# Performance work log

Measured on AMD Instinct MI355X. Metric: run time of the kernel, lower is better.

The kernel has to match this reference:

```python
import jax, jax.numpy as jnp
import numpy as np

# Config matching init_kwargs
C, H_IMG, W_IMG = 3, 224, 224
N_PATCHES = 14
PS = H_IMG // N_PATCHES            # 16
INPUT_D = C * PS * PS              # 768
HID = 768
N_HEADS = 12
DH = HID // N_HEADS                # 64
N_BLOCKS = 12
MLP_RATIO = 4
SEQ = N_PATCHES * N_PATCHES + 1    # 197
EPS = 1e-5


def _pos_embed():
    # sin on even dims, cos on odd dims, exponent uses (j - j%2)/d  (faithful to loop)
    i = jnp.arange(SEQ, dtype=jnp.float32)[:, None]
    j = jnp.arange(HID, dtype=jnp.float32)[None, :]
    expo = (j - jnp.mod(j, 2.0)) / HID
    ang = i / jnp.power(10000.0, expo)
    return jnp.where(jnp.mod(jnp.arange(HID), 2) == 0, jnp.sin(ang), jnp.cos(ang))


def setup_inputs() -> dict:
    key = jax.random.key(0)
    ks = jax.random.split(key, 16)
    s = 0.02
    d_ff = MLP_RATIO * HID
    inp = {
        'images': jax.random.normal(ks[0], (16, C, H_IMG, W_IMG), dtype=jnp.float32),
        'w_map': jax.random.normal(ks[1], (HID, INPUT_D), dtype=jnp.float32) * s,
        'b_map': jnp.zeros((HID,), dtype=jnp.float32),
        'class_token': jax.random.uniform(ks[2], (1, HID), dtype=jnp.float32),
        'pos_embed': _pos_embed(),
        'qw': jax.random.normal(ks[3], (N_BLOCKS, N_HEADS, DH, DH), dtype=jnp.float32) * s,
        'qb': jnp.zeros((N_BLOCKS, N_HEADS, DH), dtype=jnp.float32),
        'kw': jax.random.normal(ks[4], (N_BLOCKS, N_HEADS, DH, DH), dtype=jnp.float32) * s,
        'kb': jnp.zeros((N_BLOCKS, N_HEADS, DH), dtype=jnp.float32),
        'vw': jax.random.normal(ks[5], (N_BLOCKS, N_HEADS, DH, DH), dtype=jnp.float32) * s,
        'vb': jnp.zeros((N_BLOCKS, N_HEADS, DH), dtype=jnp.float32),
        'ln1_w': jnp.ones((N_BLOCKS, HID), dtype=jnp.float32),
        'ln1_b': jnp.zeros((N_BLOCKS, HID), dtype=jnp.float32),
        'ln2_w': jnp.ones((N_BLOCKS, HID), dtype=jnp.float32),
        'ln2_b': jnp.zeros((N_BLOCKS, HID), dtype=jnp.float32),
        'mlp_w1': jax.random.normal(ks[6], (N_BLOCKS, d_ff, HID), dtype=jnp.float32) * s,
        'mlp_b1': jnp.zeros((N_BLOCKS, d_ff), dtype=jnp.float32),
        'mlp_w2': jax.random.normal(ks[7], (N_BLOCKS, HID, d_ff), dtype=jnp.float32) * s,
        'mlp_b2': jnp.zeros((N_BLOCKS, HID), dtype=jnp.float32),
    }
    return inp


def _layernorm(x, w, b):
    mu = jnp.mean(x, axis=-1, keepdims=True)
    var = jnp.mean(jnp.square(x - mu), axis=-1, keepdims=True)
    return (x - mu) * jax.lax.rsqrt(var + EPS) * w + b


def _patchify(images):
    # [N,C,H,W] -> [N, np^2, C*ps*ps]; per-patch flatten order is (c, ph, pw)
    n = images.shape[0]
    x = images.reshape(n, C, N_PATCHES, PS, N_PATCHES, PS)
    x = x.transpose(0, 2, 4, 1, 3, 5)  # n, pi, pj, c, ph, pw
    return x.reshape(n, N_PATCHES * N_PATCHES, INPUT_D)


def _msa(x, qw, qb, kw, kb, vw, vb):
    # x: [B,S,D]; per-head Linear on head slices; torch Linear: y = x @ W.T + b
    b_, s_, _ = x.shape
    xh = x.reshape(b_, s_, N_HEADS, DH)
    q = jnp.einsum('bshd,hod->bsho', xh, qw) + qb
    k = jnp.einsum('bshd,hod->bsho', xh, kw) + kb
    v = jnp.einsum('bshd,hod->bsho', xh, vw) + vb
    attn = jax.nn.softmax(jnp.einsum('bsho,btho->bhst', q, k) / (DH ** 0.5), axis=-1)
    out = jnp.einsum('bhst,btho->bsho', attn, v)
    return out.reshape(b_, s_, HID)


def reference(images, w_map, b_map, class_token, pos_embed, qw, qb, kw, kb, vw, vb,
              ln1_w, ln1_b, ln2_w, ln2_b, mlp_w1, mlp_b1, mlp_w2, mlp_b2):
    patches = _patchify(images)                       # [N, 196, 768]
    tokens = patches @ w_map.T + b_map                # [N, 196, HID]
    n = tokens.shape[0]
    cls = jnp.broadcast_to(class_token[None], (n, 1, HID))
    out = jnp.concatenate([cls, tokens], axis=1) + pos_embed[None]  # [N, SEQ, HID]
    for l in range(N_BLOCKS):
        out = out + _msa(_layernorm(out, ln1_w[l], ln1_b[l]),
                         qw[l], qb[l], kw[l], kb[l], vw[l], vb[l])
        h = _layernorm(out, ln2_w[l], ln2_b[l])
        h = jax.nn.gelu(h @ mlp_w1[l].T + mlp_b1[l], approximate=False)
        out = out + (h @ mlp_w2[l].T + mlp_b2[l])
    return out
```

## Files before the change

### kernel.cpp

```cpp
#include <hip/hip_runtime.h>
#include <hip/hip_bf16.h>
#include <math.h>

typedef __attribute__((ext_vector_type(4))) float f32x4;
typedef __attribute__((ext_vector_type(8))) __bf16 bf16x8;
typedef __attribute__((ext_vector_type(8))) short short8;
typedef __attribute__((ext_vector_type(4))) unsigned short us4;
typedef __attribute__((ext_vector_type(8))) unsigned short us8;

#define B_    16
#define SEQ_  197
#define TOK_  3152
#define HID_  768
#define MPAD_ 3200
#define NP_   3136
#define DFF_  3072
#define PSZ_  (MPAD_ * HID_)
#define QKVP_ 14336
#define BHN_  192

__device__ __forceinline__ unsigned short f2bf(float x) {
  union { float f; unsigned int u; } v; v.f = x;
  unsigned int r = v.u + 0x7fffu + ((v.u >> 16) & 1u);
  return (unsigned short)(r >> 16);
}

__device__ __forceinline__ float bf2f(unsigned short u) {
  union { unsigned int i; float f; } v; v.i = ((unsigned int)u) << 16; return v.f;
}

__device__ __forceinline__ f32x4 mfma16(bf16x8 a, bf16x8 b, f32x4 c) {
  return __builtin_amdgcn_mfma_f32_16x16x32_bf16(a, b, c, 0, 0, 0);
}

__device__ __forceinline__ void cp16(const void* g, void* l) {
  __builtin_amdgcn_global_load_lds((__attribute__((address_space(1))) void*)(g),
                                   (__attribute__((address_space(3))) void*)(l),
                                   16, 0, 0);
}

__device__ __forceinline__ float gelu_f(float x) {
  float y = x * (1.5957691216f + 0.0713548162f * x * x);
  float e = __expf(y);
  float r = 1.0f / (1.0f + e);
  return x - x * r;
}

__device__ __forceinline__ void conv8(const float* __restrict__ s, unsigned short* __restrict__ d, int c) {
  const float* sp = s + (size_t)c * 8;
  f32x4 v0 = *(const f32x4*)sp;
  f32x4 v1 = *(const f32x4*)(sp + 4);
  us8 o;
  o[0] = f2bf(v0[0]); o[1] = f2bf(v0[1]); o[2] = f2bf(v0[2]); o[3] = f2bf(v0[3]);
  o[4] = f2bf(v1[0]); o[5] = f2bf(v1[1]); o[6] = f2bf(v1[2]); o[7] = f2bf(v1[3]);
  *(us8*)(d + (size_t)c * 8) = o;
}

__global__ __launch_bounds__(256) void patchcls_kernel(const float* __restrict__ img,
                                                       unsigned short* __restrict__ Pb,
                                                       const float* __restrict__ ct,
                                                       const float* __restrict__ pos,
                                                       float* __restrict__ X,
                                                       const float* __restrict__ wmap,
                                                       unsigned short* __restrict__ Wmb,
                                                       const float* __restrict__ cw1,
                                                       unsigned short* __restrict__ cd1,
                                                       const float* __restrict__ cw2,
                                                       unsigned short* __restrict__ cd2) {
  int bid = blockIdx.x;
  if (bid >= 2736) {
    int bb = bid - 2736;
    const float* s; unsigned short* d;
    if (bb < 1152) { s = cw1; d = cd1; } else { s = cw2; d = cd2; bb -= 1152; }
    conv8(s, d, bb * 256 + threadIdx.x);
    return;
  }
  if (bid >= 2448) {
    int c = (bid - 2448) * 256 + threadIdx.x;
    conv8(wmap, Wmb, c);
    return;
  }
  if (bid >= 2400) {
    int j = (bid - 2400) * 256 + threadIdx.x;
    if (j < B_ * HID_) {
      int b = j / HID_, t = j - b * HID_;
      X[(size_t)b * SEQ_ * HID_ + t] = ct[t] + pos[t];
    }
    return;
  }
  int gid = bid * 256 + threadIdx.x;
  int m = gid / 192;
  int j4 = (gid - m * 192) * 4;
  us4 o;
  if (m < NP_) {
    int n = m / 196, p = m - n * 196;
    int pi = p / 14, pj = p - pi * 14;
    int c = j4 >> 8, rem = j4 & 255, ph = rem >> 4, pw = rem & 15;
    const float* src = img + (((size_t)(n * 3 + c) * 224 + pi * 16 + ph) * 224 + pj * 16 + pw);
    f32x4 v = *(const f32x4*)src;
    o[0] = f2bf(v[0]); o[1] = f2bf(v[1]); o[2] = f2bf(v[2]); o[3] = f2bf(v[3]);
  } else {
    o[0] = 0; o[1] = 0; o[2] = 0; o[3] = 0;
  }
  *(us4*)(Pb + (size_t)m * HID_ + j4) = o;
}

__global__ __launch_bounds__(256) void convw_kernel(const float* __restrict__ s1, unsigned short* __restrict__ d1,
                                                    const float* __restrict__ s2, unsigned short* __restrict__ d2,
                                                    int nchunks) {
  int half = gridDim.x >> 1;
  int b = blockIdx.x;
  const float* s; unsigned short* d;
  if (b < half) { s = s1; d = d1; } else { s = s2; d = d2; b -= half; }
  int c = b * 256 + threadIdx.x;
  if (c >= nchunks) return;
  conv8(s, d, c);
}

__global__ __launch_bounds__(256) void gemm_embed(const unsigned short* __restrict__ A,
                                                  const unsigned short* __restrict__ Bw,
                                                  const float* __restrict__ bias,
                                                  const float* __restrict__ pos,
                                                  float* __restrict__ Xout) {
  constexpr int MI = 2, NJ = 2, BM = 64, BN = 64;
  __shared__ unsigned short As[BM * 64];
  __shared__ unsigned short Bs[BN * 64];
  const int tid = threadIdx.x;
  const int w = tid >> 6, lane = tid & 63;
  const int lr = lane & 15, kg = lane >> 4;
  int bid = blockIdx.x;
  int cpx = gridDim.x >> 3;
  int swz = (bid & 7) * cpx + (bid >> 3);
  const int by = swz / 12, bx = swz - by * 12;
  const int m0 = by * BM, n0 = bx * BN;
  const int wr = w >> 1, wc = w & 1;
  const f32x4 z4 = {0.f, 0.f, 0.f, 0.f};
  f32x4 acc[MI][NJ];
#pragma unroll
  for (int i = 0; i < MI; ++i)
#pragma unroll
    for (int j = 0; j < NJ; ++j) acc[i][j] = z4;
  for (int k0 = 0; k0 < 768; k0 += 64) {
#pragma unroll
    for (int is = 0; is < MI; ++is) {
      int chunk = is * 256 + tid;
      int row = chunk >> 3, cc = (chunk & 7) * 8;
      cp16(A + (size_t)(m0 + row) * 768 + k0 + cc, As + is * 2048 + w * 512);
    }
#pragma unroll
    for (int is = 0; is < NJ; ++is) {
      int chunk = is * 256 + tid;
      int row = chunk >> 3, cc = (chunk & 7) * 8;
      cp16(Bw + (size_t)(n0 + row) * 768 + k0 + cc, Bs + is * 2048 + w * 512);
    }
    __syncthreads();
#pragma unroll
    for (int kk = 0; kk < 64; kk += 32) {
      bf16x8 af[MI], bfr[NJ];
#pragma unroll
      for (int i = 0; i < MI; ++i)
        af[i] = *(const bf16x8*)&As[(wr * (BM / 2) + i * 16 + lr) * 64 + kk + kg * 8];
#pragma unroll
      for (int j = 0; j < NJ; ++j)
        bfr[j] = *(const bf16x8*)&Bs[(wc * (BN / 2) + j * 16 + lr) * 64 + kk + kg * 8];
#pragma unroll
      for (int i = 0; i < MI; ++i)
#pragma unroll
        for (int j = 0; j < NJ; ++j)
          acc[i][j] = mfma16(af[i], bfr[j], acc[i][j]);
    }
    __syncthreads();
  }
#pragma unroll
  for (int i = 0; i < MI; ++i) {
    int mbase = m0 + wr * (BM / 2) + i * 16 + kg * 4;
#pragma unroll
    for (int j = 0; j < NJ; ++j) {
      int col = n0 + wc * (BN / 2) + j * 16 + lr;
#pragma unroll
      for (int qr = 0; qr < 4; ++qr) {
        int m = mbase + qr;
        if (m < NP_) {
          int nimg = m / 196;
          int tok = m + nimg + 1;
          int prow = m - nimg * 196 + 1;
          Xout[(size_t)tok * HID_ + col] = acc[i][j][qr] + bias[col] + pos[(size_t)prow * HID_ + col];
        }
      }
    }
  }
}

template<int EPI, int NT>
__global__ __launch_bounds__(256, 3) void gemm4b(const unsigned short* __restrict__ A,
                                                 const unsigned short* __restrict__ Bw,
                                                 int ldk, int gx, int gy,
                                                 const float* __restrict__ bias,
                                                 unsigned short* __restrict__ Pout,
                                                 unsigned short* __restrict__ Hout) {
  __shared__ unsigned short lds3[24576];
  const int tid = threadIdx.x;
  const int wid = tid >> 6, lane = tid & 63;
  const int lr = lane & 15, kg = lane >> 4;
  const int wm = wid >> 1, wn = wid & 1;
  const int nwg = gridDim.x;
  const int q = nwg >> 3, r = nwg & 7;
  const int xcd = blockIdx.x & 7, idx = blockIdx.x >> 3;
  const int wgid = (xcd < r ? xcd * (q + 1) : r * (q + 1) + (xcd - r) * q) + idx;
  const int bx = wgid % gx;
  const int rest = wgid / gx;
  const int by = rest % gy;
  const int z = rest / gy;
  const int m0 = by * 128, n0 = bx * 128;
  const unsigned short* Abase = A + (size_t)m0 * ldk + z * (NT * 32);
  const unsigned short* Bbase = Bw + (size_t)n0 * ldk + z * (NT * 32);

  const int r0 = tid >> 2, u0 = tid & 3;
  const int r1 = 64 + r0;
  const int sk0 = (u0 ^ ((r0 >> 1) & 3)) * 8;
  const int sk1 = (u0 ^ ((r1 >> 1) & 3)) * 8;
  const int d0 = wid * 512;
  const int d1 = 2048 + wid * 512;

#pragma unroll
  for (int t = 0; t < 2; ++t) {
    unsigned short* lb = lds3 + t * 8192;
    cp16(Abase + (size_t)r0 * ldk + sk0 + t * 32, lb + d0);
    cp16(Abase + (size_t)r1 * ldk + sk1 + t * 32, lb + d1);
    cp16(Bbase + (size_t)r0 * ldk + sk0 + t * 32, lb + 4096 + d0);
    cp16(Bbase + (size_t)r1 * ldk + sk1 + t * 32, lb + 4096 + d1);
  }

  int offA[4], offB[4];
#pragma unroll
  for (int i = 0; i < 4; ++i) {
    int ra_ = wm * 64 + i * 16 + lr;
    offA[i] = ra_ * 32 + ((kg ^ ((ra_ >> 1) & 3)) * 8);
    int rb_ = wn * 64 + i * 16 + lr;
    offB[i] = rb_ * 32 + ((kg ^ ((rb_ >> 1) & 3)) * 8);
  }

  const f32x4 z4 = {0.f, 0.f, 0.f, 0.f};
  f32x4 acc[4][4];
#pragma unroll
  for (int i = 0; i < 4; ++i)
#pragma unroll
    for (int j = 0; j < 4; ++j) acc[i][j] = z4;

  int cur = 0;
#pragma unroll 1
  for (int k = 0; k < NT; ++k) {
    asm volatile("s_waitcnt vmcnt(4)" ::: "memory");
    __builtin_amdgcn_s_barrier();
    __builtin_amdgcn_sched_barrier(0);
    const unsigned short* lp = lds3 + cur * 8192;
    const int wb = (cur == 0) ? 2 : cur - 1;
    const int tn = k + 2;
    const int ts = (tn >= NT) ? tn - NT : tn;
    unsigned short* tb = lds3 + wb * 8192;
    bf16x8 af[4], bfr[4];
#pragma unroll
    for (int i = 0; i < 4; ++i)
      af[i] = *(const bf16x8*)(lp + offA[i]);
#pragma unroll
    for (int j = 0; j < 4; ++j)
      bfr[j] = *(const bf16x8*)(lp + 4096 + offB[j]);
    cp16(Abase + (size_t)r0 * ldk + sk0 + ts * 32, tb + d0);
    cp16(Abase + (size_t)r1 * ldk + sk1 + ts * 32, tb + d1);
    cp16(Bbase + (size_t)r0 * ldk + sk0 + ts * 32, tb + 4096 + d0);
    cp16(Bbase + (size_t)r1 * ldk + sk1 + ts * 32, tb + 4096 + d1);
    __builtin_amdgcn_s_setprio(1);
#pragma unroll
    for (int i = 0; i < 4; ++i)
#pragma unroll
      for (int j = 0; j < 4; ++j) acc[i][j] = mfma16(af[i], bfr[j], acc[i][j]);
    __builtin_amdgcn_s_setprio(0);
    cur = (cur == 2) ? 0 : cur + 1;
  }

#pragma unroll
  for (int i = 0; i < 4; ++i) {
    int mbase = m0 + wm * 64 + i * 16 + kg * 4;
#pragma unroll
    for (int j = 0; j < 4; ++j) {
      int col = n0 + wn * 64 + j * 16 + lr;
      float bv = (EPI == 1) ? bias[col] : 0.f;
#pragma unroll
      for (int qr = 0; qr < 4; ++qr) {
        int m = mbase + qr;
        if (m < TOK_) {
          float v = acc[i][j][qr];
          if (EPI == 1) {
            Hout[(size_t)m * 3072 + col] = f2bf(gelu_f(v + bv));
          } else {
            Pout[(size_t)z * PSZ_ + (size_t)m * 768 + col] = f2bf(v);
          }
        }
      }
    }
  }
}

template<int MODE>
__global__ __launch_bounds__(256) void ln_kernel(float* __restrict__ X,
                                                 const unsigned short* __restrict__ P, const float* __restrict__ pb,
                                                 const float* __restrict__ gw, const float* __restrict__ gb,
                                                 unsigned short* __restrict__ Y,
                                                 const float* __restrict__ cw1, unsigned short* __restrict__ cd1,
                                                 const float* __restrict__ cw2, unsigned short* __restrict__ cd2) {
  int bb = (int)blockIdx.x - 800;
  if (bb >= 0) {
    const float* s; unsigned short* d;
    if (bb < 1152) { s = cw1; d = cd1; } else { s = cw2; d = cd2; bb -= 1152; }
    conv8(s, d, bb * 256 + threadIdx.x);
    return;
  }
  int row = blockIdx.x * 4 + (threadIdx.x >> 6);
  int lane = threadIdx.x & 63;
  if (row >= MPAD_) return;
  size_t base = (size_t)row * HID_;
  if (row >= TOK_) {
    us4 zz; zz[0] = 0; zz[1] = 0; zz[2] = 0; zz[3] = 0;
#pragma unroll
    for (int i = 0; i < 3; ++i) *(us4*)(Y + base + i * 256 + lane * 4) = zz;
    return;
  }
  f32x4 xv[3];
  float s1 = 0.f, s2 = 0.f;
#pragma unroll
  for (int i = 0; i < 3; ++i) {
    int cb = i * 256 + lane * 4;
    f32x4 v = *(const f32x4*)(X + base + cb);
    if (MODE == 2) {
      const unsigned short* pp = P + base + cb;
      us4 p0 = *(const us4*)(pp);
      us4 p1 = *(const us4*)(pp + PSZ_);
      us4 p2 = *(const us4*)(pp + 2 * (size_t)PSZ_);
      us4 p3 = *(const us4*)(pp + 3 * (size_t)PSZ_);
      f32x4 bb2 = *(const f32x4*)(pb + cb);
#pragma unroll
      for (int e = 0; e < 4; ++e)
        v[e] += bf2f(p0[e]) + bf2f(p1[e]) + bf2f(p2[e]) + bf2f(p3[e]) + bb2[e];
      *(f32x4*)(X + base + cb) = v;
    }
    xv[i] = v;
    s1 += v[0] + v[1] + v[2] + v[3];
    s2 += v[0] * v[0] + v[1] * v[1] + v[2] * v[2] + v[3] * v[3];
  }
#pragma unroll
  for (int d = 1; d < 64; d <<= 1) {
    s1 += __shfl_xor(s1, d);
    s2 += __shfl_xor(s2, d);
  }
  float mu = s1 * (1.f / 768.f);
  float var = s2 * (1.f / 768.f) - mu * mu;
  float rs = rsqrtf(var + 1e-5f);
#pragma unroll
  for (int i = 0; i < 3; ++i) {
    int cb = i * 256 + lane * 4;
    us4 o;
#pragma unroll
    for (int e = 0; e < 4; ++e)
      o[e] = f2bf((xv[i][e] - mu) * rs * gw[cb + e] + gb[cb + e]);
    *(us4*)(Y + base + cb) = o;
  }
}

__global__ __launch_bounds__(256) void redfin_kernel(float* __restrict__ X, const unsigned short* __restrict__ P,
                                                     const float* __restrict__ b2) {
  int i = blockIdx.x * 256 + threadIdx.x;
  if (i >= TOK_ * 192) return;
  int m = i / 192, c4 = (i - m * 192) * 4;
  size_t off = (size_t)m * HID_ + c4;
  f32x4 v = *(const f32x4*)(X + off);
  const unsigned short* pp = P + off;
  us4 p0 = *(const us4*)(pp);
  us4 p1 = *(const us4*)(pp + PSZ_);
  us4 p2 = *(const us4*)(pp + 2 * (size_t)PSZ_);
  us4 p3 = *(const us4*)(pp + 3 * (size_t)PSZ_);
  f32x4 bb = *(const f32x4*)(b2 + c4);
#pragma unroll
  for (int e = 0; e < 4; ++e)
    v[e] += bf2f(p0[e]) + bf2f(p1[e]) + bf2f(p2[e]) + bf2f(p3[e]) + bb[e];
  *(f32x4*)(X + off) = v;
}

__device__ __forceinline__ void loadw_frags(const float* __restrict__ W, int lr, int kg, bf16x8* wf) {
#pragma unroll
  for (int j = 0; j < 4; ++j)
#pragma unroll
    for (int kk = 0; kk < 2; ++kk) {
      const float* wp = W + (j * 16 + lr) * 64 + kk * 32 + kg * 8;
      f32x4 w0 = *(const f32x4*)wp;
      f32x4 w1 = *(const f32x4*)(wp + 4);
      short8 t;
      t[0] = (short)f2bf(w0[0]); t[1] = (short)f2bf(w0[1]); t[2] = (short)f2bf(w0[2]); t[3] = (short)f2bf(w0[3]);
      t[4] = (short)f2bf(w1[0]); t[5] = (short)f2bf(w1[1]); t[6] = (short)f2bf(w1[2]); t[7] = (short)f2bf(w1[3]);
      wf[j * 2 + kk] = __builtin_bit_cast(bf16x8, t);
    }
}

__global__ __launch_bounds__(128) void qkvproj_kernel(const unsigned short* __restrict__ Y,
                                                      const float* __restrict__ qw, const float* __restrict__ qb,
                                                      const float* __restrict__ kw, const float* __restrict__ kb,
                                                      const float* __restrict__ vw, const float* __restrict__ vb,
                                                      unsigned short* __restrict__ Qo,
                                                      unsigned short* __restrict__ Ko,
                                                      unsigned short* __restrict__ Vto) {
  const int blk = blockIdx.x;
  const int half = blk & 1;
  const int bp = blk >> 1;
  const int p = bp % 3, bh = bp / 3;
  const int b = bh / 12, h = bh - b * 12;
  const int wv = threadIdx.x >> 6, lane = threadIdx.x & 63;
  const int lr = lane & 15, kg = lane >> 4;
  const int ws = half * 2 + wv;
  const float* W; const float* bs; unsigned short* out;
  if (p == 0)      { W = qw + h * 4096; bs = qb + h * 64; out = Qo; }
  else if (p == 1) { W = kw + h * 4096; bs = kb + h * 64; out = Ko; }
  else             { W = vw + h * 4096; bs = vb + h * 64; out = Vto; }
  const float scale = (p == 0) ? 0.125f : 1.0f;
  bf16x8 wf[8];
  loadw_frags(W, lr, kg, wf);
  float bj[4];
#pragma unroll
  for (int j = 0; j < 4; ++j) bj[j] = bs[j * 16 + lr];
  out += (size_t)bh * QKVP_;
  const f32x4 z4 = {0.f, 0.f, 0.f, 0.f};
  const short8 zs = {0, 0, 0, 0, 0, 0, 0, 0};
#pragma unroll
  for (int i = 0; i < 4; ++i) {
    int t = ws + 4 * i;
    if (t < 14) {
      int s = t * 16 + lr;
      bf16x8 a0 = __builtin_bit_cast(bf16x8, zs), a1 = a0;
      if (s < SEQ_) {
        const unsigned short* yp = Y + (size_t)(b * SEQ_ + s) * HID_ + h * 64 + kg * 8;
        a0 = *(const bf16x8*)yp;
        a1 = *(const bf16x8*)(yp + 32);
      }
      f32x4 acc[4] = {z4, z4, z4, z4};
#pragma unroll
      for (int j = 0; j < 4; ++j) {
        acc[j] = mfma16(a0, wf[j * 2 + 0], acc[j]);
        acc[j] = mfma16(a1, wf[j * 2 + 1], acc[j]);
      }
      if (p == 2) {
#pragma unroll
        for (int j = 0; j < 4; ++j) {
          us4 pk;
#pragma unroll
          for (int qr = 0; qr < 4; ++qr) {
            int srow = t * 16 + kg * 4 + qr;
            pk[qr] = (srow < SEQ_) ? f2bf(acc[j][qr] + bj[j]) : (unsigned short)0;
          }
          *(us4*)&out[(j * 16 + lr) * 224 + t * 16 + kg * 4] = pk;
        }
      } else {
#pragma unroll
        for (int j = 0; j < 4; ++j)
#pragma unroll
          for (int qr = 0; qr < 4; ++qr) {
            int row = t * 16 + kg * 4 + qr;
            out[row * 64 + j * 16 + lr] = f2bf((acc[j][qr] + bj[j]) * scale);
          }
      }
    }
  }
}

__global__ __launch_bounds__(64) void attn_kernel(const unsigned short* __restrict__ Qb,
                                                  const unsigned short* __restrict__ Kb,
                                                  const unsigned short* __restrict__ Vtb,
                                                  float* __restrict__ X) {
  __shared__ unsigned short plds[16 * 232];
  const int blk = blockIdx.x;
  const int qt = blk % 13, bh = blk / 13;
  const int b = bh / 12, h = bh - b * 12;
  const int lane = threadIdx.x;
  const int lr = lane & 15, kg = lane >> 4;
  const f32x4 z4 = {0.f, 0.f, 0.f, 0.f};
  const unsigned short* Qp = Qb + (size_t)bh * QKVP_;
  const unsigned short* Kp = Kb + (size_t)bh * QKVP_;
  const unsigned short* Vp = Vtb + (size_t)bh * QKVP_;
  {
    int rr = lane >> 2, c0 = 208 + (lane & 3) * 4;
    us4 zz; zz[0] = 0; zz[1] = 0; zz[2] = 0; zz[3] = 0;
    *(us4*)&plds[rr * 232 + c0] = zz;
  }
  bf16x8 aq0 = *(const bf16x8*)&Qp[(qt * 16 + lr) * 64 + kg * 8];
  bf16x8 aq1 = *(const bf16x8*)&Qp[(qt * 16 + lr) * 64 + 32 + kg * 8];
  f32x4 s[13];
#pragma unroll
  for (int nt = 0; nt < 13; ++nt) {
    const unsigned short* kp = Kp + (nt * 16 + lr) * 64 + kg * 8;
    bf16x8 b0 = *(const bf16x8*)kp;
    bf16x8 b1 = *(const bf16x8*)(kp + 32);
    f32x4 acc = mfma16(aq0, b0, z4);
    s[nt] = mfma16(aq1, b1, acc);
  }
#pragma unroll
  for (int qr = 0; qr < 4; ++qr) {
    float mx = -1e30f;
#pragma unroll
    for (int nt = 0; nt < 13; ++nt) {
      float v = (nt == 12 && lr >= 5) ? -1e30f : s[nt][qr];
      mx = fmaxf(mx, v);
    }
    mx = fmaxf(mx, __shfl_xor(mx, 1));
    mx = fmaxf(mx, __shfl_xor(mx, 2));
    mx = fmaxf(mx, __shfl_xor(mx, 4));
    mx = fmaxf(mx, __shfl_xor(mx, 8));
    float sum = 0.f;
#pragma unroll
    for (int nt = 0; nt < 13; ++nt) {
      float e = (nt == 12 && lr >= 5) ? 0.f : __expf(s[nt][qr] - mx);
      s[nt][qr] = e;
      sum += e;
    }
    sum += __shfl_xor(sum, 1);
    sum += __shfl_xor(sum, 2);
    sum += __shfl_xor(sum, 4);
    sum += __shfl_xor(sum, 8);
    float inv = 1.f / sum;
#pragma unroll
    for (int nt = 0; nt < 13; ++nt)
      plds[(kg * 4 + qr) * 232 + nt * 16 + lr] = f2bf(s[nt][qr] * inv);
  }
  asm volatile("s_waitcnt lgkmcnt(0)" ::: "memory");
  __builtin_amdgcn_sched_barrier(0);
  f32x4 ao[4] = {z4, z4, z4, z4};
#pragma unroll
  for (int kt = 0; kt < 7; ++kt) {
    bf16x8 pa = *(const bf16x8*)&plds[lr * 232 + kt * 32 + kg * 8];
#pragma unroll
    for (int j = 0; j < 4; ++j) {
      bf16x8 bv = *(const bf16x8*)&Vp[(j * 16 + lr) * 224 + kt * 32 + kg * 8];
      ao[j] = mfma16(pa, bv, ao[j]);
    }
  }
#pragma unroll
  for (int j = 0; j < 4; ++j)
#pragma unroll
    for (int qr = 0; qr < 4; ++qr) {
      int ss = qt * 16 + kg * 4 + qr;
      if (ss < SEQ_) {
        size_t xi = (size_t)(b * SEQ_ + ss) * HID_ + h * 64 + j * 16 + lr;
        X[xi] += ao[j][qr];
      }
    }
}

extern "C" void kernel_launch(void* const* d_in, const int* in_sizes, int n_in,
                              void* d_out, int out_size, void* d_ws, size_t ws_size,
                              hipStream_t stream) {
  const float* images = (const float*)d_in[0];
  const float* w_map  = (const float*)d_in[1];
  const float* b_map  = (const float*)d_in[2];
  const float* ctok   = (const float*)d_in[3];
  const float* pos    = (const float*)d_in[4];
  const float* qw   = (const float*)d_in[5];
  const float* qb   = (const float*)d_in[6];
  const float* kw   = (const float*)d_in[7];
  const float* kb   = (const float*)d_in[8];
  const float* vw   = (const float*)d_in[9];
  const float* vb   = (const float*)d_in[10];
  const float* ln1w = (const float*)d_in[11];
  const float* ln1b = (const float*)d_in[12];
  const float* ln2w = (const float*)d_in[13];
  const float* ln2b = (const float*)d_in[14];
  const float* w1   = (const float*)d_in[15];
  const float* b1   = (const float*)d_in[16];
  const float* w2   = (const float*)d_in[17];
  const float* b2   = (const float*)d_in[18];

  float* X = (float*)d_out;

  unsigned short* Y    = (unsigned short*)d_ws;
  unsigned short* Wmb  = Y + (size_t)MPAD_ * HID_;
  unsigned short* Hb   = Wmb + (size_t)768 * 768;
  unsigned short* Pp   = Hb + (size_t)MPAD_ * DFF_;
  unsigned short* Wr   = Pp + 4 * (size_t)PSZ_;

  unsigned short* Qb  = Hb;
  unsigned short* Kb2 = Hb + (size_t)BHN_ * QKVP_;
  unsigned short* Vtb = Hb + 2 * (size_t)BHN_ * QKVP_;

  const size_t L1 = (size_t)DFF_ * HID_;
  const size_t need = ((size_t)MPAD_ * HID_ + (size_t)768 * 768 + (size_t)MPAD_ * DFF_ +
                       4 * (size_t)PSZ_ + 24 * L1) * 2;
  const bool big = ws_size >= need;
  unsigned short* W1r = Wr;
  unsigned short* W2r = Wr + (big ? 12 * L1 : L1);

  patchcls_kernel<<<big ? 5040 : 2736, 256, 0, stream>>>(images, Y, ctok, pos, X,
                                                         w_map, Wmb, w1, W1r, w2, W2r);
  gemm_embed<<<600, 256, 0, stream>>>(Y, Wmb, b_map, pos, X);

  for (int l = 0; l < 12; ++l) {
    unsigned short* W1p = big ? W1r + l * L1 : W1r;
    unsigned short* W2p = big ? W2r + l * L1 : W2r;
    if (l == 0)
      ln_kernel<0><<<800, 256, 0, stream>>>(X, nullptr, nullptr,
                                            ln1w + l * 768, ln1b + l * 768, Y,
                                            nullptr, nullptr, nullptr, nullptr);
    else
      ln_kernel<2><<<800, 256, 0, stream>>>(X, Pp, b2 + (l - 1) * 768,
                                            ln1w + l * 768, ln1b + l * 768, Y,
                                            nullptr, nullptr, nullptr, nullptr);
    qkvproj_kernel<<<1152, 128, 0, stream>>>(Y,
                                             qw + (size_t)l * 49152, qb + l * 768,
                                             kw + (size_t)l * 49152, kb + l * 768,
                                             vw + (size_t)l * 49152, vb + l * 768,
                                             Qb, Kb2, Vtb);
    attn_kernel<<<2496, 64, 0, stream>>>(Qb, Kb2, Vtb, X);
    const bool cvt = big && (l < 11);
    ln_kernel<0><<<cvt ? 3104 : 800, 256, 0, stream>>>(X, nullptr, nullptr,
                                                       ln2w + l * 768, ln2b + l * 768, Y,
                                                       cvt ? w1 + (size_t)(l + 1) * L1 : nullptr,
                                                       cvt ? W1r + (size_t)(l + 1) * L1 : nullptr,
                                                       cvt ? w2 + (size_t)(l + 1) * L1 : nullptr,
                                                       cvt ? W2r + (size_t)(l + 1) * L1 : nullptr);
    if (!big)
      convw_kernel<<<2304, 256, 0, stream>>>(w1 + (size_t)l * L1, W1p,
                                             w2 + (size_t)l * L1, W2p, 294912);
    gemm4b<1, 24><<<600, 256, 0, stream>>>(Y, W1p, 768, 24, 25, b1 + l * 3072, nullptr, Hb);
    gemm4b<3, 24><<<600, 256, 0, stream>>>(Hb, W2p, 3072, 6, 25, nullptr, Pp, nullptr);
  }
  redfin_kernel<<<2364, 256, 0, stream>>>(X, Pp, b2 + 11 * 768);
}
```

Measured before the change: 1.437 ms.

## Widen MLP GEMM tiles to 128x256 with each wave owning full M

The MLP GEMM kernel changes from 128x128 to 128x256 output tiles. Each of the four waves now covers all 128 rows and a 64-column slice, which doubles the accumulators per wave and raises MFMA work per LDS B-fragment load. The launch grid is halved to 300 workgroups and occupancy drops to 2 workgroups per CU because of the larger LDS buffers and register use. With 300 workgroups on a 256-CU part there is a risk of a poor tail wave and of register pressure.

```diff
diff --git a/kernel.cpp b/kernel.cpp
--- a/kernel.cpp
+++ b/kernel.cpp
@@ -192,17 +192,16 @@
 }
 
 template<int EPI, int NT>
-__global__ __launch_bounds__(256, 3) void gemm4b(const unsigned short* __restrict__ A,
-                                                 const unsigned short* __restrict__ Bw,
-                                                 int ldk, int gx, int gy,
-                                                 const float* __restrict__ bias,
-                                                 unsigned short* __restrict__ Pout,
-                                                 unsigned short* __restrict__ Hout) {
-  __shared__ unsigned short lds3[24576];
+__global__ __launch_bounds__(256, 2) void gemm2(const unsigned short* __restrict__ A,
+                                                const unsigned short* __restrict__ Bw,
+                                                int ldk, int gx, int gy,
+                                                const float* __restrict__ bias,
+                                                unsigned short* __restrict__ Pout,
+                                                unsigned short* __restrict__ Hout) {
+  __shared__ unsigned short lds3[36864];
   const int tid = threadIdx.x;
   const int wid = tid >> 6, lane = tid & 63;
   const int lr = lane & 15, kg = lane >> 4;
-  const int wm = wid >> 1, wn = wid & 1;
   const int nwg = gridDim.x;
   const int q = nwg >> 3, r = nwg & 7;
   const int xcd = blockIdx.x & 7, idx = blockIdx.x >> 3;
@@ -211,79 +210,89 @@
   const int rest = wgid / gx;
   const int by = rest % gy;
   const int z = rest / gy;
-  const int m0 = by * 128, n0 = bx * 128;
+  const int m0 = by * 128, n0 = bx * 256;
   const unsigned short* Abase = A + (size_t)m0 * ldk + z * (NT * 32);
   const unsigned short* Bbase = Bw + (size_t)n0 * ldk + z * (NT * 32);
 
   const int r0 = tid >> 2, u0 = tid & 3;
-  const int r1 = 64 + r0;
-  const int sk0 = (u0 ^ ((r0 >> 1) & 3)) * 8;
-  const int sk1 = (u0 ^ ((r1 >> 1) & 3)) * 8;
-  const int d0 = wid * 512;
-  const int d1 = 2048 + wid * 512;
+  const int sk = (u0 ^ ((r0 >> 1) & 3)) * 8;
+  const int dA0 = wid * 512, dA1 = 2048 + wid * 512;
+
+  const f32x4 z4 = {0.f, 0.f, 0.f, 0.f};
+  f32x4 acc[8][4];
+#pragma unroll
+  for (int i = 0; i < 8; ++i)
+#pragma unroll
+    for (int j = 0; j < 4; ++j) acc[i][j] = z4;
 
 #pragma unroll
   for (int t = 0; t < 2; ++t) {
-    unsigned short* lb = lds3 + t * 8192;
-    cp16(Abase + (size_t)r0 * ldk + sk0 + t * 32, lb + d0);
-    cp16(Abase + (size_t)r1 * ldk + sk1 + t * 32, lb + d1);
-    cp16(Bbase + (size_t)r0 * ldk + sk0 + t * 32, lb + 4096 + d0);
-    cp16(Bbase + (size_t)r1 * ldk + sk1 + t * 32, lb + 4096 + d1);
-  }
-
-  int offA[4], offB[4];
-#pragma unroll
-  for (int i = 0; i < 4; ++i) {
-    int ra_ = wm * 64 + i * 16 + lr;
-    offA[i] = ra_ * 32 + ((kg ^ ((ra_ >> 1) & 3)) * 8);
-    int rb_ = wn * 64 + i * 16 + lr;
-    offB[i] = rb_ * 32 + ((kg ^ ((rb_ >> 1) & 3)) * 8);
-  }
-
-  const f32x4 z4 = {0.f, 0.f, 0.f, 0.f};
-  f32x4 acc[4][4];
-#pragma unroll
-  for (int i = 0; i < 4; ++i)
-#pragma unroll
-    for (int j = 0; j < 4; ++j) acc[i][j] = z4;
+    unsigned short* lb = lds3 + t * 12288;
+    cp16(Abase + (size_t)r0 * ldk + sk + t * 32, lb + dA0);
+    cp16(Abase + (size_t)(64 + r0) * ldk + sk + t * 32, lb + dA1);
+#pragma unroll
+    for (int c = 0; c < 4; ++c)
+      cp16(Bbase + (size_t)(c * 64 + r0) * ldk + sk + t * 32, lb + 4096 + c * 2048 + wid * 512);
+  }
+
+  int offA[8], offB[4];
+#pragma unroll
+  for (int i = 0; i < 8; ++i) {
+    int rr = i * 16 + lr;
+    offA[i] = rr * 32 + ((kg ^ ((rr >> 1) & 3)) * 8);
+  }
+#pragma unroll
+  for (int j = 0; j < 4; ++j) {
+    int rr = wid * 64 + j * 16 + lr;
+    offB[j] = 4096 + rr * 32 + ((kg ^ ((rr >> 1) & 3)) * 8);
+  }
 
   int cur = 0;
 #pragma unroll 1
   for (int k = 0; k < NT; ++k) {
-    asm volatile("s_waitcnt vmcnt(4)" ::: "memory");
+    asm volatile("s_waitcnt vmcnt(6)" ::: "memory");
     __builtin_amdgcn_s_barrier();
     __builtin_amdgcn_sched_barrier(0);
-    const unsigned short* lp = lds3 + cur * 8192;
+    const unsigned short* lp = lds3 + cur * 12288;
     const int wb = (cur == 0) ? 2 : cur - 1;
     const int tn = k + 2;
     const int ts = (tn >= NT) ? tn - NT : tn;
-    unsigned short* tb = lds3 + wb * 8192;
-    bf16x8 af[4], bfr[4];
+    unsigned short* tb = lds3 + wb * 12288;
+    bf16x8 bfr[4], af0[4];
+#pragma unroll
+    for (int j = 0; j < 4; ++j)
+      bfr[j] = *(const bf16x8*)(lp + offB[j]);
 #pragma unroll
     for (int i = 0; i < 4; ++i)
-      af[i] = *(const bf16x8*)(lp + offA[i]);
-#pragma unroll
-    for (int j = 0; j < 4; ++j)
-      bfr[j] = *(const bf16x8*)(lp + 4096 + offB[j]);
-    cp16(Abase + (size_t)r0 * ldk + sk0 + ts * 32, tb + d0);
-    cp16(Abase + (size_t)r1 * ldk + sk1 + ts * 32, tb + d1);
-    cp16(Bbase + (size_t)r0 * ldk + sk0 + ts * 32, tb + 4096 + d0);
-    cp16(Bbase + (size_t)r1 * ldk + sk1 + ts * 32, tb + 4096 + d1);
+      af0[i] = *(const bf16x8*)(lp + offA[i]);
+    cp16(Abase + (size_t)r0 * ldk + sk + ts * 32, tb + dA0);
+    cp16(Abase + (size_t)(64 + r0) * ldk + sk + ts * 32, tb + dA1);
+#pragma unroll
+    for (int c = 0; c < 4; ++c)
+      cp16(Bbase + (size_t)(c * 64 + r0) * ldk + sk + ts * 32, tb + 4096 + c * 2048 + wid * 512);
     __builtin_amdgcn_s_setprio(1);
 #pragma unroll
     for (int i = 0; i < 4; ++i)
 #pragma unroll
-      for (int j = 0; j < 4; ++j) acc[i][j] = mfma16(af[i], bfr[j], acc[i][j]);
+      for (int j = 0; j < 4; ++j) acc[i][j] = mfma16(af0[i], bfr[j], acc[i][j]);
+    bf16x8 af1[4];
+#pragma unroll
+    for (int i = 0; i < 4; ++i)
+      af1[i] = *(const bf16x8*)(lp + offA[4 + i]);
+#pragma unroll
+    for (int i = 0; i < 4; ++i)
+#pragma unroll
+      for (int j = 0; j < 4; ++j) acc[4 + i][j] = mfma16(af1[i], bfr[j], acc[4 + i][j]);
     __builtin_amdgcn_s_setprio(0);
     cur = (cur == 2) ? 0 : cur + 1;
   }
 
 #pragma unroll
-  for (int i = 0; i < 4; ++i) {
-    int mbase = m0 + wm * 64 + i * 16 + kg * 4;
+  for (int i = 0; i < 8; ++i) {
+    int mbase = m0 + i * 16 + kg * 4;
 #pragma unroll
     for (int j = 0; j < 4; ++j) {
-      int col = n0 + wn * 64 + j * 16 + lr;
+      int col = n0 + wid * 64 + j * 16 + lr;
       float bv = (EPI == 1) ? bias[col] : 0.f;
 #pragma unroll
       for (int qr = 0; qr < 4; ++qr) {
@@ -624,8 +633,8 @@
     if (!big)
       convw_kernel<<<2304, 256, 0, stream>>>(w1 + (size_t)l * L1, W1p,
                                              w2 + (size_t)l * L1, W2p, 294912);
-    gemm4b<1, 24><<<600, 256, 0, stream>>>(Y, W1p, 768, 24, 25, b1 + l * 3072, nullptr, Hb);
-    gemm4b<3, 24><<<600, 256, 0, stream>>>(Hb, W2p, 3072, 6, 25, nullptr, Pp, nullptr);
+    gemm2<1, 24><<<300, 256, 0, stream>>>(Y, W1p, 768, 12, 25, b1 + l * 3072, nullptr, Hb);
+    gemm2<3, 24><<<300, 256, 0, stream>>>(Hb, W2p, 3072, 3, 25, nullptr, Pp, nullptr);
   }
   redfin_kernel<<<2364, 256, 0, stream>>>(X, Pp, b2 + 11 * 768);
 }
```

Measured after the change: 1.585 ms. +10.3%, slower.
